# Performance work log

Measured on AMD Instinct MI355X. Metric: run time of the kernel, lower is better.

Reference implementation:

```python
import jax, jax.numpy as jnp
import numpy as np

B, F, V, L, E = 4096, 32, 100000, 20, 64  # batch, feature columns, vocab/table, bag len, emb dim


def setup_inputs() -> dict:
    key = jax.random.key(0)
    k1, k2, k3 = jax.random.split(key, 3)
    ids = jax.random.randint(k1, (B, F, L), 0, V, dtype=jnp.int64)
    lengths = jax.random.randint(k2, (B, F), 0, L + 1, dtype=jnp.int64)
    tables = jax.random.normal(k3, (F, V, E), dtype=jnp.float32) * 0.02
    return {"ids": ids, "lengths": lengths, "tables": tables}


def reference(ids, lengths, tables):
    # EmbeddingSumConcat: per-column gather + sum-pool (EmbeddingBag 'sum'),
    # concat over columns, nan-fill (empty/missing -> 0).
    F_, V_, E_ = tables.shape
    Bq, _, L_ = ids.shape
    flat = tables.reshape(F_ * V_, E_)
    offs = jnp.arange(F_, dtype=ids.dtype)[None, :, None] * V_
    emb = flat[ids + offs]                                   # [B, F, L, E] gather
    mask = (jnp.arange(L_) < lengths[..., None]).astype(emb.dtype)  # [B, F, L]
    pooled = jnp.einsum('bfle,bfl->bfe', emb, mask)          # masked sum-pool
    out = pooled.reshape(Bq, F_ * E_)                        # concat columns
    return jnp.nan_to_num(out)                               # use_nan_fill=True
```

## Files before the change

kernel.cpp:

```cpp
#include <hip/hip_runtime.h>


#define BB 4096
#define FF 32
#define VV 100000
#define LL 20
#define EE 64

__global__ __launch_bounds__(256) void emb_bag_sum_kernel(
    const int* __restrict__ ids,
    const int* __restrict__ lengths,
    const float* __restrict__ tables,
    float* __restrict__ out)
{
    const int wave = threadIdx.x >> 6;
    const int lane = threadIdx.x & 63;
    const int bag  = (blockIdx.x << 2) + wave;
    const int f    = bag & (FF - 1);

    const int len = lengths[bag];
    const int* __restrict__ idp = ids + bag * LL;
    const float* __restrict__ tab = tables + (size_t)f * (VV * EE);

    int myid = (lane < LL) ? idp[lane] : 0;
    const int lastl = (len > 0) ? (len - 1) : 0;

    int off[LL];
#pragma unroll
    for (int l = 0; l < LL; ++l) {
        const int sl = (l < len) ? l : lastl;
        const int id = __shfl(myid, sl);
        off[l] = (id << 6) + lane;
    }

    float v[LL];
#pragma unroll
    for (int l = 0; l < LL; ++l) v[l] = tab[off[l]];

    float acc = 0.0f;
#pragma unroll
    for (int l = 0; l < LL; ++l) acc += (l < len) ? v[l] : 0.0f;

    out[bag * EE + lane] = acc;
}

extern "C" void kernel_launch(void* const* d_in, const int* in_sizes, int n_in,
                              void* d_out, int out_size, void* d_ws, size_t ws_size,
                              hipStream_t stream) {
    const int*   ids     = (const int*)d_in[0];
    const int*   lengths = (const int*)d_in[1];
    const float* tables  = (const float*)d_in[2];
    float*       out     = (float*)d_out;

    const int n_bags = BB * FF;
    const int blocks = n_bags / 4;
    emb_bag_sum_kernel<<<blocks, 256, 0, stream>>>(ids, lengths, tables, out);
}
```

Before: 937.1 us.

## Vectorize row gathers with float4 across four bag slots and skip empty slots

Each wave now splits into four 16-lane groups that each load one table row as float4, so one wave handles four bag positions per load round across five rounds. Loads are skipped for whole rounds beyond the wave-uniform bag length, which avoids fetching rows for padded positions. Partial sums from the four groups are combined with xor shuffles and written as float4 by the first 16 lanes. This trades fewer, wider memory instructions and skipped padding reads for extra cross-lane shuffle work.

```diff
diff --git a/kernel.cpp b/kernel.cpp
--- a/kernel.cpp
+++ b/kernel.cpp
@@ -6,6 +6,7 @@
 #define VV 100000
 #define LL 20
 #define EE 64
+#define NR 5
 
 __global__ __launch_bounds__(256) void emb_bag_sum_kernel(
     const int* __restrict__ ids,
@@ -17,31 +18,53 @@
     const int lane = threadIdx.x & 63;
     const int bag  = (blockIdx.x << 2) + wave;
     const int f    = bag & (FF - 1);
+    const int g    = lane >> 4;
+    const int e4   = (lane & 15) << 2;
 
-    const int len = lengths[bag];
+    const int len  = lengths[bag];
+    const int lenu = __builtin_amdgcn_readfirstlane(len);
     const int* __restrict__ idp = ids + bag * LL;
     const float* __restrict__ tab = tables + (size_t)f * (VV * EE);
 
     int myid = (lane < LL) ? idp[lane] : 0;
-    const int lastl = (len > 0) ? (len - 1) : 0;
+    const int lastl = (lenu > 0) ? (lenu - 1) : 0;
 
-    int off[LL];
+    int sid[NR];
 #pragma unroll
-    for (int l = 0; l < LL; ++l) {
-        const int sl = (l < len) ? l : lastl;
-        const int id = __shfl(myid, sl);
-        off[l] = (id << 6) + lane;
+    for (int r = 0; r < NR; ++r) {
+        const int l  = 4 * r + g;
+        const int sl = (l < lenu) ? l : lastl;
+        sid[r] = __shfl(myid, sl);
     }
 
-    float v[LL];
+    float4 v[NR];
 #pragma unroll
-    for (int l = 0; l < LL; ++l) v[l] = tab[off[l]];
+    for (int r = 0; r < NR; ++r) {
+        if (4 * r < lenu) {
+            v[r] = *(const float4*)(tab + ((sid[r] << 6) + e4));
+        }
+    }
 
-    float acc = 0.0f;
+    float4 acc = make_float4(0.0f, 0.0f, 0.0f, 0.0f);
 #pragma unroll
-    for (int l = 0; l < LL; ++l) acc += (l < len) ? v[l] : 0.0f;
+    for (int r = 0; r < NR; ++r) {
+        if (4 * r < lenu) {
+            const bool m = (4 * r + g) < lenu;
+            acc.x += m ? v[r].x : 0.0f;
+            acc.y += m ? v[r].y : 0.0f;
+            acc.z += m ? v[r].z : 0.0f;
+            acc.w += m ? v[r].w : 0.0f;
+        }
+    }
 
-    out[bag * EE + lane] = acc;
+    acc.x += __shfl_xor(acc.x, 16); acc.y += __shfl_xor(acc.y, 16);
+    acc.z += __shfl_xor(acc.z, 16); acc.w += __shfl_xor(acc.w, 16);
+    acc.x += __shfl_xor(acc.x, 32); acc.y += __shfl_xor(acc.y, 32);
+    acc.z += __shfl_xor(acc.z, 32); acc.w += __shfl_xor(acc.w, 32);
+
+    if (lane < 16) {
+        *(float4*)(out + (size_t)bag * EE + e4) = acc;
+    }
 }
 
 extern "C" void kernel_launch(void* const* d_in, const int* in_sizes, int n_in,
```

Result: no change. 935.7 us (-0.2%).
